# Performance work log

Hardware: AMD Instinct MI355X
Metric: run time of the kernel (lower is better)

The kernel has to match this reference:

```python
import jax, jax.numpy as jnp
import numpy as np

N_NODES = 100000
N_EDGES = 800000
HIDDEN = 64
N_LAYERS = 3
N_TYPES = 64
LN_EPS = 1e-5


def setup_inputs() -> dict:
    key = jax.random.key(0)
    ks = jax.random.split(key, 10)
    type_indices = jax.random.randint(ks[0], (N_NODES,), 0, N_TYPES)
    edges = jax.random.randint(ks[1], (N_EDGES, 2), 0, N_NODES)
    s = 1.0 / np.sqrt(2 * HIDDEN)
    return {
        "type_indices": type_indices,
        "edges": edges,
        "embed_table": jax.random.normal(ks[2], (N_TYPES, HIDDEN), jnp.float32),
        "msg_w": jax.random.uniform(ks[3], (N_LAYERS, 2 * HIDDEN, HIDDEN), jnp.float32, -s, s),
        "msg_b": jax.random.uniform(ks[4], (N_LAYERS, HIDDEN), jnp.float32, -s, s),
        "upd_w": jax.random.uniform(ks[5], (N_LAYERS, 2 * HIDDEN, HIDDEN), jnp.float32, -s, s),
        "upd_b": jax.random.uniform(ks[6], (N_LAYERS, HIDDEN), jnp.float32, -s, s),
        "ln_g": jnp.ones((N_LAYERS, HIDDEN), jnp.float32),
        "ln_b": jnp.zeros((N_LAYERS, HIDDEN), jnp.float32),
    }


def _layer_norm(h, g, b):
    mu = h.mean(-1, keepdims=True)
    var = ((h - mu) ** 2).mean(-1, keepdims=True)
    return (h - mu) * jax.lax.rsqrt(var + LN_EPS) * g + b


def reference(type_indices, edges, embed_table, msg_w, msg_b, upd_w, upd_b, ln_g, ln_b):
    N = type_indices.shape[0]
    src, tgt = edges[:, 0], edges[:, 1]
    x = embed_table[type_indices]                          # [N, D]
    for i in range(N_LAYERS):
        # per-edge: gather src/tgt features, linear + relu message
        m_in = jnp.concatenate([x[src], x[tgt]], axis=-1)  # [E, 2D]
        msg = jax.nn.relu(m_in @ msg_w[i] + msg_b[i])      # [E, D]
        # scatter-mean by target node
        agg = jax.ops.segment_sum(msg, tgt, num_segments=N)
        cnt = jax.ops.segment_sum(jnp.ones_like(tgt, dtype=x.dtype), tgt, num_segments=N)
        agg = agg / jnp.clip(cnt, 1.0)[:, None]
        # residual update + LayerNorm
        u = jax.nn.relu(jnp.concatenate([x, agg], axis=-1) @ upd_w[i] + upd_b[i])
        x = _layer_norm(u + x, ln_g[i], ln_b[i])
    # global readout: mean + max pooling
    return jnp.concatenate([x.mean(axis=0), x.max(axis=0)])
```

## Files before the change

### kernel.cpp

```cpp
#include <hip/hip_runtime.h>
#include <hip/hip_fp16.h>
#include <math.h>

#define NND 100000
#define NED 800000
#define NLAY 3
#define BSH 9
#define NBKT ((NND + 511) / 512)
#define CAP 8192
static constexpr float LNEPS = 1e-5f;

typedef __attribute__((ext_vector_type(8))) short short8;
typedef __attribute__((ext_vector_type(4))) float floatx4;

__device__ __forceinline__ short f2bf(float f) {
    unsigned u = __float_as_uint(f);
    u += 0x7fffu + ((u >> 16) & 1u);
    return (short)(u >> 16);
}
__device__ __forceinline__ float bf2f(short s) {
    return __uint_as_float(((unsigned)(unsigned short)s) << 16);
}

__device__ __forceinline__ void load_h8(const __half* p, float* f) {
    uint4 v = *(const uint4*)p;
    unsigned a[4] = {v.x, v.y, v.z, v.w};
#pragma unroll
    for (int k = 0; k < 4; k++) {
        __half2 h = *(__half2*)&a[k];
        float2 g = __half22float2(h);
        f[2 * k] = g.x; f[2 * k + 1] = g.y;
    }
}

__global__ void k_init(int* __restrict__ gtail, float* __restrict__ rsum, unsigned* __restrict__ rmax) {
    int gt = blockIdx.x * blockDim.x + threadIdx.x;
    if (gt < NBKT) gtail[gt] = gt * CAP;
    if (gt >= 256 && gt < 320) { rsum[gt - 256] = 0.f; rmax[gt - 256] = 0u; }
}

__global__ __launch_bounds__(256) void k_bscatter(const int2* __restrict__ e, int* __restrict__ gtail,
                                                  long long* __restrict__ tmp) {
    __shared__ int cnt[NBKT], chunk[NBKT], cur[NBKT];
    const int T = 4096;
    int ntile = (NED + T - 1) / T;
    for (int tile = blockIdx.x; tile < ntile; tile += gridDim.x) {
        int base = tile * T;
        int t = threadIdx.x;
        for (int i = t; i < NBKT; i += 256) { cnt[i] = 0; cur[i] = 0; }
        __syncthreads();
        int2 ed[16]; int bk[16];
#pragma unroll
        for (int i = 0; i < 16; i++) {
            int idx = base + i * 256 + t;
            if (idx < NED) {
                ed[i] = e[idx];
                bk[i] = ((unsigned)ed[i].y) >> BSH;
                atomicAdd(&cnt[bk[i]], 1);
            } else bk[i] = -1;
        }
        __syncthreads();
        for (int i = t; i < NBKT; i += 256) if (cnt[i]) chunk[i] = atomicAdd(&gtail[i], cnt[i]);
        __syncthreads();
#pragma unroll
        for (int i = 0; i < 16; i++) {
            if (bk[i] >= 0) {
                int r = atomicAdd(&cur[bk[i]], 1);
                tmp[(size_t)chunk[bk[i]] + r] =
                    ((long long)(unsigned)ed[i].y << 32) | (unsigned)ed[i].x;
            }
        }
        __syncthreads();
    }
}

__global__ __launch_bounds__(512) void k_bfinish(const long long* __restrict__ tmp, const int* __restrict__ gtail,
                                                 int* __restrict__ rowb, int* __restrict__ degv,
                                                 int* __restrict__ srcs) {
    __shared__ int ld[512];
    __shared__ int lcur[512];
    int b = blockIdx.x, t = threadIdx.x;
    int node0 = b << BSH;
    int nn = min(512, NND - node0);
    int ebase = b * CAP, eend = gtail[b];
    ld[t] = 0;
    __syncthreads();
    for (int i = ebase + t; i < eend; i += 512) {
        int tgt = (int)(tmp[i] >> 32);
        atomicAdd(&ld[tgt - node0], 1);
    }
    __syncthreads();
    int v = ld[t];
    for (int off = 1; off < 512; off <<= 1) {
        int u = (t >= off) ? ld[t - off] : 0;
        __syncthreads();
        ld[t] += u;
        __syncthreads();
    }
    int exc = ld[t] - v;
    if (t < nn) { rowb[node0 + t] = ebase + exc; degv[node0 + t] = v; }
    lcur[t] = exc;
    __syncthreads();
    for (int i = ebase + t; i < eend; i += 512) {
        long long pk = tmp[i];
        int tgt = (int)(pk >> 32);
        int src = (int)(pk & 0xffffffffll);
        int p = atomicAdd(&lcur[tgt - node0], 1);
        srcs[ebase + p] = src;
    }
}

__global__ void k_prep(const float* __restrict__ msg_w, const float* __restrict__ upd_w,
                       short* __restrict__ wmsg, short* __restrict__ wupd) {
    int t = blockIdx.x * blockDim.x + threadIdx.x;
    if (t >= 2 * NLAY * 8192) return;
    int which = t / (NLAY * 8192);
    int e = t % (NLAY * 8192);
    int l = e >> 13, idx = e & 8191;
    int j = idx & 7, lane = (idx >> 3) & 63, hi = idx >> 9;
    int lm = lane & 15, quad = lane >> 4;
    if (which == 0) {
        int ks = hi & 1, nt = hi >> 1;
        int n = nt * 16 + lm, k = ks * 32 + quad * 8 + j;
        float v = (n < 64) ? msg_w[(size_t)l * 8192 + k * 64 + n]
                           : msg_w[(size_t)l * 8192 + (64 + k) * 64 + (n - 64)];
        wmsg[e] = f2bf(v);
    } else {
        int ks = hi & 3, nt = hi >> 2;
        int n = nt * 16 + lm, k = ks * 32 + quad * 8 + j;
        wupd[e] = f2bf(upd_w[(size_t)l * 8192 + k * 64 + n]);
    }
}

__global__ __launch_bounds__(256) void k_pq(const int* __restrict__ ty, const float* __restrict__ tab,
                                            const short* __restrict__ wb, const float* __restrict__ bg,
                                            __half* __restrict__ P16, __half* __restrict__ Q16,
                                            short* __restrict__ x16) {
    __shared__ __half outs[64 * 136];
    int wv = threadIdx.x >> 6, lane = threadIdx.x & 63;
    int lm = lane & 15, quad = lane >> 4;
    int nbase = blockIdx.x * 64;
    int m = nbase + wv * 16 + lm;
    short8 a[2];
    if (m < NND) {
        const float* tr = tab + ty[m] * 64;
#pragma unroll
        for (int ks = 0; ks < 2; ks++) {
            float4 v0 = *(const float4*)(tr + ks * 32 + quad * 8);
            float4 v1 = *(const float4*)(tr + ks * 32 + quad * 8 + 4);
            short8 av;
            av[0] = f2bf(v0.x); av[1] = f2bf(v0.y); av[2] = f2bf(v0.z); av[3] = f2bf(v0.w);
            av[4] = f2bf(v1.x); av[5] = f2bf(v1.y); av[6] = f2bf(v1.z); av[7] = f2bf(v1.w);
            a[ks] = av;
            *(short8*)(x16 + (size_t)m * 64 + ks * 32 + quad * 8) = av;
        }
    } else {
#pragma unroll
        for (int ks = 0; ks < 2; ks++) { short8 z; for (int j = 0; j < 8; j++) z[j] = 0; a[ks] = z; }
    }
    floatx4 acc[8];
#pragma unroll
    for (int nt = 0; nt < 8; nt++) acc[nt] = (floatx4){0.f, 0.f, 0.f, 0.f};
#pragma unroll
    for (int nt = 0; nt < 8; nt++) {
        short8 b0 = *(const short8*)(wb + (size_t)((nt * 2 + 0) * 64 + lane) * 8);
        short8 b1 = *(const short8*)(wb + (size_t)((nt * 2 + 1) * 64 + lane) * 8);
        acc[nt] = __builtin_amdgcn_mfma_f32_16x16x32_bf16(a[0], b0, acc[nt], 0, 0, 0);
        acc[nt] = __builtin_amdgcn_mfma_f32_16x16x32_bf16(a[1], b1, acc[nt], 0, 0, 0);
    }
    float bq[4];
#pragma unroll
    for (int nt = 0; nt < 4; nt++) bq[nt] = bg[nt * 16 + lm];
#pragma unroll
    for (int reg = 0; reg < 4; reg++) {
        int rown = wv * 16 + quad * 4 + reg;
#pragma unroll
        for (int nt = 0; nt < 4; nt++)
            outs[rown * 136 + nt * 16 + lm] = __float2half(acc[nt][reg]);
#pragma unroll
        for (int nt = 4; nt < 8; nt++)
            outs[rown * 136 + 64 + (nt - 4) * 16 + lm] = __float2half(acc[nt][reg] + bq[nt - 4]);
    }
    __syncthreads();
    int t = threadIdx.x;
#pragma unroll
    for (int r = 0; r < 4; r++) {
        int s = r * 256 + t;
        int node = s >> 4, seg = s & 15;
        int gn = nbase + node;
        if (gn < NND) {
            uint4 v = *(const uint4*)(outs + node * 136 + seg * 8);
            __half* dst = (seg < 8) ? (P16 + (size_t)gn * 64 + seg * 8)
                                    : (Q16 + (size_t)gn * 64 + (seg - 8) * 8);
            *(uint4*)dst = v;
        }
    }
}

__global__ __launch_bounds__(256, 4) void k_aggupd(short* __restrict__ x16, const __half* __restrict__ P16,
                                                   const __half* __restrict__ Q16,
                                                   const int* __restrict__ rowb, const int* __restrict__ degv,
                                                   const int* __restrict__ srcs,
                                                   const short* __restrict__ wu, const float* __restrict__ ub,
                                                   const float* __restrict__ lg, const float* __restrict__ lb,
                                                   const short* __restrict__ wm, const float* __restrict__ bgn,
                                                   __half* __restrict__ Pout, __half* __restrict__ Qout, int last) {
    __shared__ float aggs[64 * 68];
    int t = threadIdx.x, w = t >> 6, lane = t & 63;

    {
        int ln = lane >> 2, fq = lane & 3, c0 = fq * 16;
        int bn = w * 16 + ln;
        int wid = blockIdx.x * 64 + bn;
        float acc[16];
#pragma unroll
        for (int k = 0; k < 16; k++) acc[k] = 0.f;
        if (wid < NND) {
            int beg = rowb[wid], dg = degv[wid], end = beg + dg;
            float qv[16];
            load_h8(Q16 + (size_t)wid * 64 + c0, qv);
            load_h8(Q16 + (size_t)wid * 64 + c0 + 8, qv + 8);
            int e = beg;
            int n0 = 0, n1 = 0, n2 = 0, n3 = 0;
            if (e + 4 <= end) { n0 = srcs[e]; n1 = srcs[e + 1]; n2 = srcs[e + 2]; n3 = srcs[e + 3]; }
            while (e + 4 <= end) {
                int c0s = n0, c1s = n1, c2s = n2, c3s = n3;
                int en = e + 4;
                if (en + 4 <= end) { n0 = srcs[en]; n1 = srcs[en + 1]; n2 = srcs[en + 2]; n3 = srcs[en + 3]; }
                float f0[16], f1[16], f2[16], f3[16];
                load_h8(P16 + (size_t)c0s * 64 + c0, f0); load_h8(P16 + (size_t)c0s * 64 + c0 + 8, f0 + 8);
                load_h8(P16 + (size_t)c1s * 64 + c0, f1); load_h8(P16 + (size_t)c1s * 64 + c0 + 8, f1 + 8);
                load_h8(P16 + (size_t)c2s * 64 + c0, f2); load_h8(P16 + (size_t)c2s * 64 + c0 + 8, f2 + 8);
                load_h8(P16 + (size_t)c3s * 64 + c0, f3); load_h8(P16 + (size_t)c3s * 64 + c0 + 8, f3 + 8);
#pragma unroll
                for (int k = 0; k < 16; k++) {
                    acc[k] += fmaxf(f0[k] + qv[k], 0.f) + fmaxf(f1[k] + qv[k], 0.f);
                    acc[k] += fmaxf(f2[k] + qv[k], 0.f) + fmaxf(f3[k] + qv[k], 0.f);
                }
                e = en;
            }
            for (; e < end; e++) {
                int s = srcs[e];
                float f0[16];
                load_h8(P16 + (size_t)s * 64 + c0, f0);
                load_h8(P16 + (size_t)s * 64 + c0 + 8, f0 + 8);
#pragma unroll
                for (int k = 0; k < 16; k++) acc[k] += fmaxf(f0[k] + qv[k], 0.f);
            }
            float inv = 1.f / fmaxf((float)dg, 1.f);
#pragma unroll
            for (int s4 = 0; s4 < 4; s4++)
                *(float4*)(aggs + bn * 68 + c0 + s4 * 4) =
                    make_float4(acc[s4 * 4] * inv, acc[s4 * 4 + 1] * inv,
                                acc[s4 * 4 + 2] * inv, acc[s4 * 4 + 3] * inv);
        } else {
#pragma unroll
            for (int s4 = 0; s4 < 4; s4++)
                *(float4*)(aggs + bn * 68 + c0 + s4 * 4) = make_float4(0.f, 0.f, 0.f, 0.f);
        }
    }

    int lm = lane & 15, quad = lane >> 4;
    int gmbase = blockIdx.x * 64 + w * 16;
    int m = gmbase + lm;
    int bm = w * 16 + lm;

    short8 a[4];
#pragma unroll
    for (int ks = 0; ks < 2; ks++) {
        if (m < NND) a[ks] = *(const short8*)(x16 + (size_t)m * 64 + ks * 32 + quad * 8);
        else { short8 z; for (int j = 0; j < 8; j++) z[j] = 0; a[ks] = z; }
    }
#pragma unroll
    for (int ks = 2; ks < 4; ks++) {
        const float* p = aggs + bm * 68 + (ks - 2) * 32 + quad * 8;
        float4 v0 = *(const float4*)p;
        float4 v1 = *(const float4*)(p + 4);
        float xv[8] = {v0.x, v0.y, v0.z, v0.w, v1.x, v1.y, v1.z, v1.w};
        short8 av;
#pragma unroll
        for (int j = 0; j < 8; j++) av[j] = f2bf(xv[j]);
        a[ks] = av;
    }
    floatx4 acc4[4];
#pragma unroll
    for (int nt = 0; nt < 4; nt++) acc4[nt] = (floatx4){0.f, 0.f, 0.f, 0.f};
#pragma unroll
    for (int nt = 0; nt < 4; nt++) {
#pragma unroll
        for (int ks = 0; ks < 4; ks++) {
            short8 b = *(const short8*)(wu + (size_t)((nt * 4 + ks) * 64 + lane) * 8);
            acc4[nt] = __builtin_amdgcn_mfma_f32_16x16x32_bf16(a[ks], b, acc4[nt], 0, 0, 0);
        }
    }
    float ubv[4], lgv[4], lbv[4];
#pragma unroll
    for (int nt = 0; nt < 4; nt++) {
        int col = nt * 16 + lm;
        ubv[nt] = ub[col]; lgv[nt] = lg[col]; lbv[nt] = lb[col];
    }
#pragma unroll
    for (int reg = 0; reg < 4; reg++) {
        int rown = w * 16 + quad * 4 + reg;
        int gn = blockIdx.x * 64 + rown;
        bool ok = gn < NND;
        float h[4];
#pragma unroll
        for (int nt = 0; nt < 4; nt++) {
            float xv = ok ? bf2f(x16[(size_t)gn * 64 + nt * 16 + lm]) : 0.f;
            float u = fmaxf(acc4[nt][reg] + ubv[nt], 0.f);
            h[nt] = u + xv;
        }
        float s1 = h[0] + h[1] + h[2] + h[3];
        float s2 = h[0] * h[0] + h[1] * h[1] + h[2] * h[2] + h[3] * h[3];
#pragma unroll
        for (int off = 1; off < 16; off *= 2) {
            s1 += __shfl_xor(s1, off);
            s2 += __shfl_xor(s2, off);
        }
        float mu = s1 * (1.f / 64.f);
        float var = s2 * (1.f / 64.f) - mu * mu;
        float rs = rsqrtf(var + LNEPS);
#pragma unroll
        for (int nt = 0; nt < 4; nt++) {
            float res = (h[nt] - mu) * rs * lgv[nt] + lbv[nt];
            if (ok) x16[(size_t)gn * 64 + nt * 16 + lm] = f2bf(res);
            aggs[rown * 68 + nt * 16 + lm] = res;
        }
    }

    if (!last) {
        __half* hs = (__half*)aggs;
        short8 na[2];
#pragma unroll
        for (int ks = 0; ks < 2; ks++) {
            const float* p = aggs + bm * 68 + ks * 32 + quad * 8;
            float4 v0 = *(const float4*)p;
            float4 v1 = *(const float4*)(p + 4);
            float xv[8] = {v0.x, v0.y, v0.z, v0.w, v1.x, v1.y, v1.z, v1.w};
            short8 av;
#pragma unroll
            for (int j = 0; j < 8; j++) av[j] = f2bf(xv[j]);
            na[ks] = av;
        }
        floatx4 c8[8];
#pragma unroll
        for (int nt = 0; nt < 8; nt++) c8[nt] = (floatx4){0.f, 0.f, 0.f, 0.f};
#pragma unroll
        for (int nt = 0; nt < 8; nt++) {
            short8 b0 = *(const short8*)(wm + (size_t)((nt * 2 + 0) * 64 + lane) * 8);
            short8 b1 = *(const short8*)(wm + (size_t)((nt * 2 + 1) * 64 + lane) * 8);
            c8[nt] = __builtin_amdgcn_mfma_f32_16x16x32_bf16(na[0], b0, c8[nt], 0, 0, 0);
            c8[nt] = __builtin_amdgcn_mfma_f32_16x16x32_bf16(na[1], b1, c8[nt], 0, 0, 0);
        }
        float bq[4];
#pragma unroll
        for (int nt = 0; nt < 4; nt++) bq[nt] = bgn[nt * 16 + lm];
#pragma unroll
        for (int reg = 0; reg < 4; reg++) {
            int rown = w * 16 + quad * 4 + reg;
#pragma unroll
            for (int nt = 0; nt < 4; nt++)
                hs[rown * 136 + nt * 16 + lm] = __float2half(c8[nt][reg]);
#pragma unroll
            for (int nt = 4; nt < 8; nt++)
                hs[rown * 136 + 64 + (nt - 4) * 16 + lm] = __float2half(c8[nt][reg] + bq[nt - 4]);
        }
#pragma unroll
        for (int pass = 0; pass < 4; pass++) {
            int idx = pass * 64 + lane;
            int nd = idx >> 4, seg = idx & 15;
            int rown = w * 16 + nd;
            int gn = blockIdx.x * 64 + rown;
            if (gn < NND) {
                uint4 v = *(const uint4*)(hs + rown * 136 + seg * 8);
                __half* dst = (seg < 8) ? (Pout + (size_t)gn * 64 + seg * 8)
                                        : (Qout + (size_t)gn * 64 + (seg - 8) * 8);
                *(uint4*)dst = v;
            }
        }
    }
}

__global__ void k_reduce(const short* __restrict__ x16, float* __restrict__ rsum, unsigned* __restrict__ rmax) {
    __shared__ float sb[256];
    __shared__ float mb[256];
    int t = threadIdx.x;
    int j = t & 63, g = t >> 6;
    float s = 0.f, m = -3.402823466e38f;
    for (int r = blockIdx.x * 4 + g; r < NND; r += gridDim.x * 4) {
        float v = bf2f(x16[(size_t)r * 64 + j]);
        s += v;
        m = fmaxf(m, v);
    }
    sb[t] = s; mb[t] = m; __syncthreads();
    if (t < 64) {
        s = sb[t] + sb[t + 64] + sb[t + 128] + sb[t + 192];
        m = fmaxf(fmaxf(mb[t], mb[t + 64]), fmaxf(mb[t + 128], mb[t + 192]));
        atomicAdd(&rsum[j], s);
        unsigned b = __float_as_uint(m);
        unsigned enc = (b & 0x80000000u) ? ~b : (b | 0x80000000u);
        atomicMax(&rmax[j], enc);
    }
}

__global__ void k_fin(const float* __restrict__ rsum, const unsigned* __restrict__ rmax, float* __restrict__ out) {
    int t = threadIdx.x;
    if (t < 64) {
        out[t] = rsum[t] * (1.f / (float)NND);
    } else if (t < 128) {
        unsigned u = rmax[t - 64];
        unsigned b = (u & 0x80000000u) ? (u & 0x7fffffffu) : ~u;
        out[t] = __uint_as_float(b);
    }
}

extern "C" void kernel_launch(void* const* d_in, const int* in_sizes, int n_in,
                              void* d_out, int out_size, void* d_ws, size_t ws_size,
                              hipStream_t stream) {
    const int* ty      = (const int*)d_in[0];
    const int* ed      = (const int*)d_in[1];
    const float* tab   = (const float*)d_in[2];
    const float* msg_w = (const float*)d_in[3];
    const float* msg_b = (const float*)d_in[4];
    const float* upd_w = (const float*)d_in[5];
    const float* upd_b = (const float*)d_in[6];
    const float* ln_g  = (const float*)d_in[7];
    const float* ln_b  = (const float*)d_in[8];
    float* out = (float*)d_out;

    char* w = (char*)d_ws;
    auto alloc = [&](size_t sz) { char* p = w; w += (sz + 255) & ~(size_t)255; return p; };
    short* x16     = (short*)alloc((size_t)NND * 64 * 2);
    __half* P0     = (__half*)alloc((size_t)NND * 64 * 2);
    __half* Q0     = (__half*)alloc((size_t)NND * 64 * 2);
    __half* P1     = (__half*)alloc((size_t)NND * 64 * 2);
    __half* Q1     = (__half*)alloc((size_t)NND * 64 * 2);
    long long* tmp = (long long*)alloc((size_t)NBKT * CAP * 8);
    int* srcs      = (int*)alloc((size_t)NBKT * CAP * 4);
    int* rowb      = (int*)alloc((size_t)NND * 4);
    int* degv      = (int*)alloc((size_t)NND * 4);
    int* gtail     = (int*)alloc(256 * 4);
    float* rsum    = (float*)alloc(64 * 4);
    unsigned* rmax = (unsigned*)alloc(64 * 4);
    short* wmsg    = (short*)alloc((size_t)NLAY * 8192 * 2);
    short* wupd    = (short*)alloc((size_t)NLAY * 8192 * 2);

    k_init<<<2, 256, 0, stream>>>(gtail, rsum, rmax);
    k_prep<<<(2 * NLAY * 8192 + 255) / 256, 256, 0, stream>>>(msg_w, upd_w, wmsg, wupd);
    k_bscatter<<<(NED + 4095) / 4096, 256, 0, stream>>>((const int2*)ed, gtail, tmp);
    k_bfinish<<<NBKT, 512, 0, stream>>>(tmp, gtail, rowb, degv, srcs);

    k_pq<<<(NND + 63) / 64, 256, 0, stream>>>(ty, tab, wmsg, msg_b, P0, Q0, x16);

    const int GB = (NND + 63) / 64;
    k_aggupd<<<GB, 256, 0, stream>>>(x16, P0, Q0, rowb, degv, srcs,
                                     wupd + 0 * 8192, upd_b + 0, ln_g + 0, ln_b + 0,
                                     wmsg + 1 * 8192, msg_b + 64, P1, Q1, 0);
    k_aggupd<<<GB, 256, 0, stream>>>(x16, P1, Q1, rowb, degv, srcs,
                                     wupd + 1 * 8192, upd_b + 64, ln_g + 64, ln_b + 64,
                                     wmsg + 2 * 8192, msg_b + 128, P0, Q0, 0);
    k_aggupd<<<GB, 256, 0, stream>>>(x16, P0, Q0, rowb, degv, srcs,
                                     wupd + 2 * 8192, upd_b + 128, ln_g + 128, ln_b + 128,
                                     wmsg + 2 * 8192, msg_b + 128, P1, Q1, 1);

    k_reduce<<<256, 256, 0, stream>>>(x16, rsum, rmax);
    k_fin<<<1, 128, 0, stream>>>(rsum, rmax, out);
}
```

Baseline: 256.9 us.

## Store gathered message projections in fp8 and fuse readout into last layer

The per-source message projection P, which is gathered once per edge, is now stored as fp8 (e4m3) instead of fp16, halving the bytes read in the edge aggregation loop. The target-side projection Q stays fp16. The final layer also computes the column sum and max pooling in-kernel with shuffles, shared atomics and global atomics, removing the separate reduce kernel and the last x16 write and re-read. The risk is precision loss from fp8 quantization of the message terms, which may exceed tolerance.

```diff
diff --git a/kernel.cpp b/kernel.cpp
--- a/kernel.cpp
+++ b/kernel.cpp
@@ -12,6 +12,7 @@
 
 typedef __attribute__((ext_vector_type(8))) short short8;
 typedef __attribute__((ext_vector_type(4))) float floatx4;
+typedef __attribute__((ext_vector_type(2))) float floatx2;
 
 __device__ __forceinline__ short f2bf(float f) {
     unsigned u = __float_as_uint(f);
@@ -31,6 +32,22 @@
         float2 g = __half22float2(h);
         f[2 * k] = g.x; f[2 * k + 1] = g.y;
     }
+}
+
+__device__ __forceinline__ void load_f8x16(const unsigned char* p, float* f) {
+    uint4 v = *(const uint4*)p;
+    unsigned a[4] = {v.x, v.y, v.z, v.w};
+#pragma unroll
+    for (int k = 0; k < 4; k++) {
+        floatx2 lo = __builtin_amdgcn_cvt_pk_f32_fp8(a[k], false);
+        floatx2 hi = __builtin_amdgcn_cvt_pk_f32_fp8(a[k], true);
+        f[4 * k + 0] = lo[0]; f[4 * k + 1] = lo[1];
+        f[4 * k + 2] = hi[0]; f[4 * k + 3] = hi[1];
+    }
+}
+__device__ __forceinline__ unsigned char f32_to_fp8(float v) {
+    int r = __builtin_amdgcn_cvt_pk_fp8_f32(v, v, 0, false);
+    return (unsigned char)(r & 0xff);
 }
 
 __global__ void k_init(int* __restrict__ gtail, float* __restrict__ rsum, unsigned* __restrict__ rmax) {
@@ -134,9 +151,9 @@
 
 __global__ __launch_bounds__(256) void k_pq(const int* __restrict__ ty, const float* __restrict__ tab,
                                             const short* __restrict__ wb, const float* __restrict__ bg,
-                                            __half* __restrict__ P16, __half* __restrict__ Q16,
+                                            unsigned char* __restrict__ P8, __half* __restrict__ Q16,
                                             short* __restrict__ x16) {
-    __shared__ __half outs[64 * 136];
+    __shared__ unsigned char outs[64 * 272];
     int wv = threadIdx.x >> 6, lane = threadIdx.x & 63;
     int lm = lane & 15, quad = lane >> 4;
     int nbase = blockIdx.x * 64;
@@ -174,39 +191,50 @@
 #pragma unroll
     for (int reg = 0; reg < 4; reg++) {
         int rown = wv * 16 + quad * 4 + reg;
+        unsigned char* rb = outs + rown * 272;
 #pragma unroll
         for (int nt = 0; nt < 4; nt++)
-            outs[rown * 136 + nt * 16 + lm] = __float2half(acc[nt][reg]);
+            rb[nt * 16 + lm] = f32_to_fp8(acc[nt][reg]);
 #pragma unroll
         for (int nt = 4; nt < 8; nt++)
-            outs[rown * 136 + 64 + (nt - 4) * 16 + lm] = __float2half(acc[nt][reg] + bq[nt - 4]);
-    }
-    __syncthreads();
-    int t = threadIdx.x;
-#pragma unroll
-    for (int r = 0; r < 4; r++) {
-        int s = r * 256 + t;
-        int node = s >> 4, seg = s & 15;
-        int gn = nbase + node;
+            *(__half*)(rb + 64 + (((nt - 4) * 16 + lm) << 1)) = __float2half(acc[nt][reg] + bq[nt - 4]);
+    }
+#pragma unroll
+    for (int pass = 0; pass < 3; pass++) {
+        int idx = pass * 64 + lane;
+        int ndl = (idx * 171) >> 11;
+        int seg = idx - ndl * 12;
+        int rown = wv * 16 + ndl;
+        int gn = nbase + rown;
         if (gn < NND) {
-            uint4 v = *(const uint4*)(outs + node * 136 + seg * 8);
-            __half* dst = (seg < 8) ? (P16 + (size_t)gn * 64 + seg * 8)
-                                    : (Q16 + (size_t)gn * 64 + (seg - 8) * 8);
-            *(uint4*)dst = v;
-        }
-    }
-}
-
-__global__ __launch_bounds__(256, 4) void k_aggupd(short* __restrict__ x16, const __half* __restrict__ P16,
+            int off = (seg < 4) ? seg * 16 : 64 + (seg - 4) * 16;
+            uint4 v = *(const uint4*)(outs + rown * 272 + off);
+            if (seg < 4) *(uint4*)(P8 + (size_t)gn * 64 + seg * 16) = v;
+            else *(uint4*)((char*)Q16 + (size_t)gn * 128 + (seg - 4) * 16) = v;
+        }
+    }
+}
+
+__global__ __launch_bounds__(256, 4) void k_aggupd(short* __restrict__ x16, const unsigned char* __restrict__ P8,
                                                    const __half* __restrict__ Q16,
                                                    const int* __restrict__ rowb, const int* __restrict__ degv,
                                                    const int* __restrict__ srcs,
                                                    const short* __restrict__ wu, const float* __restrict__ ub,
                                                    const float* __restrict__ lg, const float* __restrict__ lb,
                                                    const short* __restrict__ wm, const float* __restrict__ bgn,
-                                                   __half* __restrict__ Pout, __half* __restrict__ Qout, int last) {
+                                                   unsigned char* __restrict__ Pout, __half* __restrict__ Qout,
+                                                   float* __restrict__ rsum, unsigned* __restrict__ rmax,
+                                                   int last) {
     __shared__ float aggs[64 * 68];
+    __shared__ float redsum[64];
+    __shared__ unsigned redmax[64];
     int t = threadIdx.x, w = t >> 6, lane = t & 63;
+
+    if (last) {
+        if (t < 64) redsum[t] = 0.f;
+        else if (t < 128) redmax[t - 64] = 0u;
+        __syncthreads();
+    }
 
     {
         int ln = lane >> 2, fq = lane & 3, c0 = fq * 16;
@@ -228,10 +256,10 @@
                 int en = e + 4;
                 if (en + 4 <= end) { n0 = srcs[en]; n1 = srcs[en + 1]; n2 = srcs[en + 2]; n3 = srcs[en + 3]; }
                 float f0[16], f1[16], f2[16], f3[16];
-                load_h8(P16 + (size_t)c0s * 64 + c0, f0); load_h8(P16 + (size_t)c0s * 64 + c0 + 8, f0 + 8);
-                load_h8(P16 + (size_t)c1s * 64 + c0, f1); load_h8(P16 + (size_t)c1s * 64 + c0 + 8, f1 + 8);
-                load_h8(P16 + (size_t)c2s * 64 + c0, f2); load_h8(P16 + (size_t)c2s * 64 + c0 + 8, f2 + 8);
-                load_h8(P16 + (size_t)c3s * 64 + c0, f3); load_h8(P16 + (size_t)c3s * 64 + c0 + 8, f3 + 8);
+                load_f8x16(P8 + (size_t)c0s * 64 + c0, f0);
+                load_f8x16(P8 + (size_t)c1s * 64 + c0, f1);
+                load_f8x16(P8 + (size_t)c2s * 64 + c0, f2);
+                load_f8x16(P8 + (size_t)c3s * 64 + c0, f3);
 #pragma unroll
                 for (int k = 0; k < 16; k++) {
                     acc[k] += fmaxf(f0[k] + qv[k], 0.f) + fmaxf(f1[k] + qv[k], 0.f);
@@ -242,8 +270,7 @@
             for (; e < end; e++) {
                 int s = srcs[e];
                 float f0[16];
-                load_h8(P16 + (size_t)s * 64 + c0, f0);
-                load_h8(P16 + (size_t)s * 64 + c0 + 8, f0 + 8);
+                load_f8x16(P8 + (size_t)s * 64 + c0, f0);
 #pragma unroll
                 for (int k = 0; k < 16; k++) acc[k] += fmaxf(f0[k] + qv[k], 0.f);
             }
@@ -299,6 +326,8 @@
         int col = nt * 16 + lm;
         ubv[nt] = ub[col]; lgv[nt] = lg[col]; lbv[nt] = lb[col];
     }
+    float csum[4] = {0.f, 0.f, 0.f, 0.f};
+    float cmax[4] = {-3.402823466e38f, -3.402823466e38f, -3.402823466e38f, -3.402823466e38f};
 #pragma unroll
     for (int reg = 0; reg < 4; reg++) {
         int rown = w * 16 + quad * 4 + reg;
@@ -324,13 +353,41 @@
 #pragma unroll
         for (int nt = 0; nt < 4; nt++) {
             float res = (h[nt] - mu) * rs * lgv[nt] + lbv[nt];
-            if (ok) x16[(size_t)gn * 64 + nt * 16 + lm] = f2bf(res);
-            aggs[rown * 68 + nt * 16 + lm] = res;
-        }
-    }
-
-    if (!last) {
-        __half* hs = (__half*)aggs;
+            if (!last) {
+                if (ok) x16[(size_t)gn * 64 + nt * 16 + lm] = f2bf(res);
+                aggs[rown * 68 + nt * 16 + lm] = res;
+            } else if (ok) {
+                csum[nt] += res;
+                cmax[nt] = fmaxf(cmax[nt], res);
+            }
+        }
+    }
+
+    if (last) {
+#pragma unroll
+        for (int nt = 0; nt < 4; nt++) {
+            csum[nt] += __shfl_xor(csum[nt], 16);
+            csum[nt] += __shfl_xor(csum[nt], 32);
+            cmax[nt] = fmaxf(cmax[nt], __shfl_xor(cmax[nt], 16));
+            cmax[nt] = fmaxf(cmax[nt], __shfl_xor(cmax[nt], 32));
+        }
+        if (quad == 0) {
+#pragma unroll
+            for (int nt = 0; nt < 4; nt++) {
+                atomicAdd(&redsum[nt * 16 + lm], csum[nt]);
+                unsigned b = __float_as_uint(cmax[nt]);
+                unsigned enc = (b & 0x80000000u) ? ~b : (b | 0x80000000u);
+                atomicMax(&redmax[nt * 16 + lm], enc);
+            }
+        }
+        __syncthreads();
+        if (t < 64) atomicAdd(&rsum[t], redsum[t]);
+        else if (t < 128) atomicMax(&rmax[t - 64], redmax[t - 64]);
+        return;
+    }
+
+    {
+        unsigned char* bs = (unsigned char*)aggs;
         short8 na[2];
 #pragma unroll
         for (int ks = 0; ks < 2; ks++) {
@@ -359,48 +416,28 @@
 #pragma unroll
         for (int reg = 0; reg < 4; reg++) {
             int rown = w * 16 + quad * 4 + reg;
+            unsigned char* rb = bs + rown * 272;
 #pragma unroll
             for (int nt = 0; nt < 4; nt++)
-                hs[rown * 136 + nt * 16 + lm] = __float2half(c8[nt][reg]);
+                rb[nt * 16 + lm] = f32_to_fp8(c8[nt][reg]);
 #pragma unroll
             for (int nt = 4; nt < 8; nt++)
-                hs[rown * 136 + 64 + (nt - 4) * 16 + lm] = __float2half(c8[nt][reg] + bq[nt - 4]);
-        }
-#pragma unroll
-        for (int pass = 0; pass < 4; pass++) {
+                *(__half*)(rb + 64 + (((nt - 4) * 16 + lm) << 1)) = __float2half(c8[nt][reg] + bq[nt - 4]);
+        }
+#pragma unroll
+        for (int pass = 0; pass < 3; pass++) {
             int idx = pass * 64 + lane;
-            int nd = idx >> 4, seg = idx & 15;
-            int rown = w * 16 + nd;
+            int ndl = (idx * 171) >> 11;
+            int seg = idx - ndl * 12;
+            int rown = w * 16 + ndl;
             int gn = blockIdx.x * 64 + rown;
             if (gn < NND) {
-                uint4 v = *(const uint4*)(hs + rown * 136 + seg * 8);
-                __half* dst = (seg < 8) ? (Pout + (size_t)gn * 64 + seg * 8)
-                                        : (Qout + (size_t)gn * 64 + (seg - 8) * 8);
-                *(uint4*)dst = v;
+                int off = (seg < 4) ? seg * 16 : 64 + (seg - 4) * 16;
+                uint4 v = *(const uint4*)(bs + rown * 272 + off);
+                if (seg < 4) *(uint4*)(Pout + (size_t)gn * 64 + seg * 16) = v;
+                else *(uint4*)((char*)Qout + (size_t)gn * 128 + (seg - 4) * 16) = v;
             }
         }
-    }
-}
-
-__global__ void k_reduce(const short* __restrict__ x16, float* __restrict__ rsum, unsigned* __restrict__ rmax) {
-    __shared__ float sb[256];
-    __shared__ float mb[256];
-    int t = threadIdx.x;
-    int j = t & 63, g = t >> 6;
-    float s = 0.f, m = -3.402823466e38f;
-    for (int r = blockIdx.x * 4 + g; r < NND; r += gridDim.x * 4) {
-        float v = bf2f(x16[(size_t)r * 64 + j]);
-        s += v;
-        m = fmaxf(m, v);
-    }
-    sb[t] = s; mb[t] = m; __syncthreads();
-    if (t < 64) {
-        s = sb[t] + sb[t + 64] + sb[t + 128] + sb[t + 192];
-        m = fmaxf(fmaxf(mb[t], mb[t + 64]), fmaxf(mb[t + 128], mb[t + 192]));
-        atomicAdd(&rsum[j], s);
-        unsigned b = __float_as_uint(m);
-        unsigned enc = (b & 0x80000000u) ? ~b : (b | 0x80000000u);
-        atomicMax(&rmax[j], enc);
     }
 }
 
@@ -431,20 +468,20 @@
 
     char* w = (char*)d_ws;
     auto alloc = [&](size_t sz) { char* p = w; w += (sz + 255) & ~(size_t)255; return p; };
-    short* x16     = (short*)alloc((size_t)NND * 64 * 2);
-    __half* P0     = (__half*)alloc((size_t)NND * 64 * 2);
-    __half* Q0     = (__half*)alloc((size_t)NND * 64 * 2);
-    __half* P1     = (__half*)alloc((size_t)NND * 64 * 2);
-    __half* Q1     = (__half*)alloc((size_t)NND * 64 * 2);
-    long long* tmp = (long long*)alloc((size_t)NBKT * CAP * 8);
-    int* srcs      = (int*)alloc((size_t)NBKT * CAP * 4);
-    int* rowb      = (int*)alloc((size_t)NND * 4);
-    int* degv      = (int*)alloc((size_t)NND * 4);
-    int* gtail     = (int*)alloc(256 * 4);
-    float* rsum    = (float*)alloc(64 * 4);
-    unsigned* rmax = (unsigned*)alloc(64 * 4);
-    short* wmsg    = (short*)alloc((size_t)NLAY * 8192 * 2);
-    short* wupd    = (short*)alloc((size_t)NLAY * 8192 * 2);
+    short* x16         = (short*)alloc((size_t)NND * 64 * 2);
+    unsigned char* P0  = (unsigned char*)alloc((size_t)NND * 64);
+    unsigned char* P1  = (unsigned char*)alloc((size_t)NND * 64);
+    __half* Q0         = (__half*)alloc((size_t)NND * 64 * 2);
+    __half* Q1         = (__half*)alloc((size_t)NND * 64 * 2);
+    long long* tmp     = (long long*)alloc((size_t)NBKT * CAP * 8);
+    int* srcs          = (int*)alloc((size_t)NBKT * CAP * 4);
+    int* rowb          = (int*)alloc((size_t)NND * 4);
+    int* degv          = (int*)alloc((size_t)NND * 4);
+    int* gtail         = (int*)alloc(256 * 4);
+    float* rsum        = (float*)alloc(64 * 4);
+    unsigned* rmax     = (unsigned*)alloc(64 * 4);
+    short* wmsg        = (short*)alloc((size_t)NLAY * 8192 * 2);
+    short* wupd        = (short*)alloc((size_t)NLAY * 8192 * 2);
 
     k_init<<<2, 256, 0, stream>>>(gtail, rsum, rmax);
     k_prep<<<(2 * NLAY * 8192 + 255) / 256, 256, 0, stream>>>(msg_w, upd_w, wmsg, wupd);
@@ -456,14 +493,13 @@
     const int GB = (NND + 63) / 64;
     k_aggupd<<<GB, 256, 0, stream>>>(x16, P0, Q0, rowb, degv, srcs,
                                      wupd + 0 * 8192, upd_b + 0, ln_g + 0, ln_b + 0,
-                                     wmsg + 1 * 8192, msg_b + 64, P1, Q1, 0);
+                                     wmsg + 1 * 8192, msg_b + 64, P1, Q1, rsum, rmax, 0);
     k_aggupd<<<GB, 256, 0, stream>>>(x16, P1, Q1, rowb, degv, srcs,
                                      wupd + 1 * 8192, upd_b + 64, ln_g + 64, ln_b + 64,
-                                     wmsg + 2 * 8192, msg_b + 128, P0, Q0, 0);
+                                     wmsg + 2 * 8192, msg_b + 128, P0, Q0, rsum, rmax, 0);
     k_aggupd<<<GB, 256, 0, stream>>>(x16, P0, Q0, rowb, degv, srcs,
                                      wupd + 2 * 8192, upd_b + 128, ln_g + 128, ln_b + 128,
-                                     wmsg + 2 * 8192, msg_b + 128, P1, Q1, 1);
-
-    k_reduce<<<256, 256, 0, stream>>>(x16, rsum, rmax);
+                                     wmsg + 2 * 8192, msg_b + 128, P1, Q1, rsum, rmax, 1);
+
     k_fin<<<1, 128, 0, stream>>>(rsum, rmax, out);
 }
```

Result: faster. 244.3 us (-4.9%).
